# Kernel optimization log

Hardware: AMD Instinct MI355X
Metric: run time of the kernel (lower is better)

## Reference

```python
import jax, jax.numpy as jnp
import numpy as np

B, NP, P, DIM = 128, 64, 128, 512
DST, DCONV, DEPTH = 16, 4, 2
DIN = 2 * DIM          # expand * dim
DTR = DIM // 16        # dt_rank
NCLS = 32


def setup_inputs() -> dict:
    key = jax.random.key(0)
    ks = jax.random.split(key, 12)
    r = lambda k, shape, s=0.02: jax.random.normal(k, shape, jnp.float32) * s
    A_log = jnp.log(jnp.arange(1, DST + 1, dtype=jnp.float32))  # S4D-real init
    return {
        "series": jax.random.normal(ks[0], (B, NP * P), jnp.float32),
        "seg_w": r(ks[1], (NP, P, DIM)),
        "seg_b": jnp.zeros((NP, DIM), jnp.float32),
        "ln_g": jnp.ones((NP, DIM), jnp.float32),
        "ln_b": jnp.zeros((NP, DIM), jnp.float32),
        "in_proj_w": r(ks[2], (DEPTH, 2 * DIN, DIM)),
        "conv_w": r(ks[3], (DEPTH, DIN, DCONV), 0.1),
        "conv_b": jnp.zeros((DEPTH, DIN), jnp.float32),
        "x_proj_w": r(ks[4], (DEPTH, DTR + 2 * DST, DIN)),
        "dt_proj_w": r(ks[5], (DEPTH, DIN, DTR), 0.1),
        "dt_proj_b": r(ks[6], (DEPTH, DIN), 0.5) - 4.0,  # small softplus(dt)
        "A_log": jnp.tile(A_log, (DEPTH, DIN, 1)),
        "D": jnp.ones((DEPTH, DIN), jnp.float32),
        "out_proj_w": r(ks[7], (DEPTH, DIM, DIN)),
        "head_ln_g": jnp.ones((NP * DIM,), jnp.float32),
        "head_ln_b": jnp.zeros((NP * DIM,), jnp.float32),
        "head_w": r(ks[8], (NCLS, NP * DIM)),
        "head_b": jnp.zeros((NCLS,), jnp.float32),
    }


def _layernorm(x, g, b, eps=1e-5):
    mu = x.mean(-1, keepdims=True)
    var = x.var(-1, keepdims=True)
    return (x - mu) / jnp.sqrt(var + eps) * g + b


def _mamba_block(x, wi, cw, cb, wx, wdt, bdt, A_log, Dp, wo):
    # x: [b, l, DIM]
    b, l, _ = x.shape
    xz = jnp.einsum('bld,ed->ble', x, wi)            # [b, l, 2*DIN]
    u, z = jnp.split(xz, 2, axis=-1)
    # depthwise causal conv1d (kernel DCONV, left pad DCONV-1)
    up = jnp.pad(u, ((0, 0), (DCONV - 1, 0), (0, 0)))
    uc = sum(up[:, k:k + l, :] * cw[:, k] for k in range(DCONV)) + cb
    uc = jax.nn.silu(uc)
    x_dbl = jnp.einsum('bld,ed->ble', uc, wx)        # [b, l, DTR+2*DST]
    dt, Bm, Cm = jnp.split(x_dbl, [DTR, DTR + DST], axis=-1)
    delta = jax.nn.softplus(jnp.einsum('blr,dr->bld', dt, wdt) + bdt)  # [b,l,DIN]
    A = -jnp.exp(A_log)                               # [DIN, DST]

    def step(h, inp):
        d_t, B_t, C_t, u_t = inp                      # [b,DIN],[b,DST],[b,DST],[b,DIN]
        dA = jnp.exp(d_t[:, :, None] * A)             # [b, DIN, DST]
        h = dA * h + (d_t * u_t)[:, :, None] * B_t[:, None, :]
        y = jnp.einsum('bdn,bn->bd', h, C_t)
        return h, y

    xs = (delta.transpose(1, 0, 2), Bm.transpose(1, 0, 2),
          Cm.transpose(1, 0, 2), uc.transpose(1, 0, 2))
    h0 = jnp.zeros((b, DIN, DST), x.dtype)
    _, ys = jax.lax.scan(step, h0, xs)                # [l, b, DIN]
    y = ys.transpose(1, 0, 2) + uc * Dp
    y = y * jax.nn.silu(z)
    return jnp.einsum('bld,ed->ble', y, wo)           # [b, l, DIM]


def _forward(series, seg_w, seg_b, ln_g, ln_b, in_proj_w, conv_w, conv_b,
             x_proj_w, dt_proj_w, dt_proj_b, A_log, D, out_proj_w,
             head_ln_g, head_ln_b, head_w, head_b):
    b = series.shape[0]
    x = series.reshape(b, NP, P)                      # equal-size pathway split
    x = jnp.einsum('bnp,npd->bnd', x, seg_w) + seg_b  # per-pathway Linear
    x = _layernorm(x, ln_g, ln_b)                     # per-pathway LayerNorm
    for i in range(DEPTH):                            # stacked Mamba (no residual)
        x = _mamba_block(x, in_proj_w[i], conv_w[i], conv_b[i], x_proj_w[i],
                         dt_proj_w[i], dt_proj_b[i], A_log[i], D[i], out_proj_w[i])
    x = x.reshape(b, NP * DIM)
    x = _layernorm(x, head_ln_g, head_ln_b)
    return x @ head_w.T + head_b


def reference(series, seg_w, seg_b, ln_g, ln_b, in_proj_w, conv_w, conv_b,
              x_proj_w, dt_proj_w, dt_proj_b, A_log, D, out_proj_w,
              head_ln_g, head_ln_b, head_w, head_b):
    return _forward(series, seg_w, seg_b, ln_g, ln_b, in_proj_w, conv_w, conv_b,
                    x_proj_w, dt_proj_w, dt_proj_b, A_log, D, out_proj_w,
                    head_ln_g, head_ln_b, head_w, head_b)
```

## Files before the change

### kernel.cpp

```cpp
#include <hip/hip_runtime.h>

typedef unsigned short u16;
typedef unsigned int   u32;
typedef __attribute__((ext_vector_type(8))) short short8;
typedef __attribute__((ext_vector_type(4))) float floatx4;

static __device__ __forceinline__ float silu_f(float x){
  return x / (1.f + __expf(-x));
}
static __device__ __forceinline__ float bfu2f(u16 u){
  union { u32 i; float f; } v; v.i = ((u32)u) << 16; return v.f;
}
static __device__ __forceinline__ u16 f2bfu(float f){
  union { float f; u32 i; } v; v.f = f;
  u32 x = v.i;
  u32 r = (x + 0x7fffu + ((x >> 16) & 1u)) >> 16;
  return (u16)r;
}
static __device__ __forceinline__ float softplus_f(float v){
  return fmaxf(v, 0.f) + log1pf(__expf(-fabsf(v)));
}

constexpr int cB = 128, cNP = 64, cP = 128, cDIM = 512, cDIN = 1024;
constexpr int cDST = 16, cDTR = 32, cNCLS = 32;
constexpr int cBL = cB * cNP;
constexpr int cXZ = 2 * cDIN;
constexpr long cPSTR = (long)cBL * 64;

__global__ __launch_bounds__(256) void k_f2bf_all(
    const float* __restrict__ s0, u16* __restrict__ d0, int n0,
    const float* __restrict__ s1, u16* __restrict__ d1, int n1,
    const float* __restrict__ s2, u16* __restrict__ d2, int n2,
    const float* __restrict__ s3, u16* __restrict__ d3, int n3,
    const float* __restrict__ s4, u16* __restrict__ d4, int n4)
{
  int i = blockIdx.x * 256 + threadIdx.x;
  const float* s; u16* d;
  if (i < n0) { s = s0; d = d0; }
  else {
    i -= n0;
    if (i < n1) { s = s1; d = d1; }
    else {
      i -= n1;
      if (i < n2) { s = s2; d = d2; }
      else {
        i -= n2;
        if (i < n3) { s = s3; d = d3; }
        else {
          i -= n3;
          if (i >= n4) return;
          s = s4; d = d4;
        }
      }
    }
  }
  const size_t off = (size_t)i * 4;
  float4 v = *(const float4*)(s + off);
  ushort4 o;
  o.x = f2bfu(v.x); o.y = f2bfu(v.y); o.z = f2bfu(v.z); o.w = f2bfu(v.w);
  *(ushort4*)(d + off) = o;
}

__global__ __launch_bounds__(256) void k_segT(
    const float* __restrict__ src, u16* __restrict__ dst)
{
  const int n = blockIdx.z;
  const int p0 = blockIdx.x * 32;
  const int d0 = blockIdx.y * 32;
  const int tx = threadIdx.x & 31;
  const int ty = threadIdx.x >> 5;
  __shared__ float t[32][33];
#pragma unroll
  for (int r = 0; r < 4; ++r)
    t[ty + r * 8][tx] = src[(size_t)n * (cP * cDIM) + (p0 + ty + r * 8) * cDIM + d0 + tx];
  __syncthreads();
#pragma unroll
  for (int r = 0; r < 4; ++r)
    dst[(size_t)n * (cDIM * cP) + (d0 + ty + r * 8) * cP + p0 + tx] =
        f2bfu(t[tx][ty + r * 8]);
}

template<int AMODE, int EPI>
__global__ __launch_bounds__(256) void k_gemm_mfma(
    const void* __restrict__ Av, int lda,
    const u16* __restrict__ W,
    float* __restrict__ C, int ldc,
    u16* __restrict__ Cb, int ldcb,
    const float* __restrict__ bias,
    int K, long azs, long wzs, long czs,
    const float* __restrict__ cwp, const float* __restrict__ cbp,
    u16* __restrict__ ucp)
{
  constexpr int LDT = 40;
  constexpr int SU_LD = 136;
  constexpr int GEMM_SM = 2 * 128 * LDT;
  constexpr int SM_SZ = (EPI == 2) ? (128 * SU_LD) : GEMM_SM;
  __shared__ __align__(16) u16 smem[SM_SZ];
  u16* As = smem;
  u16* Ws = smem + 128 * LDT;

  const int bz = blockIdx.z;
  const u16* Wz = W + (size_t)bz * wzs;

  const int tid = threadIdx.x;
  const int bm = blockIdx.x * 128;
  const int bn = blockIdx.y * 128;
  const int wave = tid >> 6;
  const int lane = tid & 63;
  const int wm = (wave & 1) * 64;
  const int wn = (wave >> 1) * 64;
  const int l15 = lane & 15;
  const int quad = lane >> 4;

  floatx4 acc[4][4];
#pragma unroll
  for (int i = 0; i < 4; ++i)
#pragma unroll
    for (int j = 0; j < 4; ++j) acc[i][j] = (floatx4){0.f, 0.f, 0.f, 0.f};

  const int r0 = tid >> 2;
  const int c0 = (tid & 3) * 8;

  const float* Af = (const float*)Av + (AMODE == 1 ? (size_t)bz * azs : 0);
  const u16*   Ab = (const u16*)Av + (AMODE == 0 ? (size_t)bz * azs : 0);

  float4 fa0, fb0, fa1, fb1;
  short8 ra0, ra1, rw0, rw1;

  if constexpr (AMODE == 1) {
    const float* p0 = Af + (size_t)(bm + r0) * lda + c0;
    const float* p1 = Af + (size_t)(bm + r0 + 64) * lda + c0;
    fa0 = *(const float4*)p0; fb0 = *(const float4*)(p0 + 4);
    fa1 = *(const float4*)p1; fb1 = *(const float4*)(p1 + 4);
  } else if constexpr (AMODE == 0) {
    ra0 = *(const short8*)(Ab + (size_t)(bm + r0)      * lda + c0);
    ra1 = *(const short8*)(Ab + (size_t)(bm + r0 + 64) * lda + c0);
  }
  rw0 = *(const short8*)(Wz + (size_t)(bn + r0)      * K + c0);
  rw1 = *(const short8*)(Wz + (size_t)(bn + r0 + 64) * K + c0);

  for (int k0 = 0; k0 < K; k0 += 32) {
    if constexpr (AMODE == 1) {
      short8 s0, s1;
      s0[0] = (short)f2bfu(fa0.x); s0[1] = (short)f2bfu(fa0.y);
      s0[2] = (short)f2bfu(fa0.z); s0[3] = (short)f2bfu(fa0.w);
      s0[4] = (short)f2bfu(fb0.x); s0[5] = (short)f2bfu(fb0.y);
      s0[6] = (short)f2bfu(fb0.z); s0[7] = (short)f2bfu(fb0.w);
      s1[0] = (short)f2bfu(fa1.x); s1[1] = (short)f2bfu(fa1.y);
      s1[2] = (short)f2bfu(fa1.z); s1[3] = (short)f2bfu(fa1.w);
      s1[4] = (short)f2bfu(fb1.x); s1[5] = (short)f2bfu(fb1.y);
      s1[6] = (short)f2bfu(fb1.z); s1[7] = (short)f2bfu(fb1.w);
      *(short8*)&As[r0 * LDT + c0] = s0;
      *(short8*)&As[(r0 + 64) * LDT + c0] = s1;
    } else if constexpr (AMODE == 0) {
      *(short8*)&As[r0 * LDT + c0] = ra0;
      *(short8*)&As[(r0 + 64) * LDT + c0] = ra1;
    } else {
      const float* base = (const float*)Av;
#pragma unroll
      for (int h = 0; h < 2; ++h) {
        const float* p = base + (size_t)(bm + r0 + h * 64) * 64 + c0;
        float4 a = *(const float4*)p;
        float4 b = *(const float4*)(p + 4);
#pragma unroll
        for (int kc = 1; kc < 4; ++kc) {
          const float* q = p + (size_t)kc * azs;
          float4 va = *(const float4*)q, vb = *(const float4*)(q + 4);
          a.x += va.x; a.y += va.y; a.z += va.z; a.w += va.w;
          b.x += vb.x; b.y += vb.y; b.z += vb.z; b.w += vb.w;
        }
        short8 st;
        st[0] = (short)f2bfu(a.x); st[1] = (short)f2bfu(a.y);
        st[2] = (short)f2bfu(a.z); st[3] = (short)f2bfu(a.w);
        st[4] = (short)f2bfu(b.x); st[5] = (short)f2bfu(b.y);
        st[6] = (short)f2bfu(b.z); st[7] = (short)f2bfu(b.w);
        *(short8*)&As[(r0 + h * 64) * LDT + c0] = st;
      }
    }
    *(short8*)&Ws[r0 * LDT + c0] = rw0;
    *(short8*)&Ws[(r0 + 64) * LDT + c0] = rw1;
    __syncthreads();

    const int kn = k0 + 32;
    if (kn < K) {
      if constexpr (AMODE == 1) {
        const float* p0 = Af + (size_t)(bm + r0) * lda + kn + c0;
        const float* p1 = Af + (size_t)(bm + r0 + 64) * lda + kn + c0;
        fa0 = *(const float4*)p0; fb0 = *(const float4*)(p0 + 4);
        fa1 = *(const float4*)p1; fb1 = *(const float4*)(p1 + 4);
      } else if constexpr (AMODE == 0) {
        ra0 = *(const short8*)(Ab + (size_t)(bm + r0)      * lda + kn + c0);
        ra1 = *(const short8*)(Ab + (size_t)(bm + r0 + 64) * lda + kn + c0);
      }
      rw0 = *(const short8*)(Wz + (size_t)(bn + r0)      * K + kn + c0);
      rw1 = *(const short8*)(Wz + (size_t)(bn + r0 + 64) * K + kn + c0);
    }

    short8 af[4], bf[4];
#pragma unroll
    for (int i = 0; i < 4; ++i)
      af[i] = *(const short8*)&As[(wm + i * 16 + l15) * LDT + quad * 8];
#pragma unroll
    for (int j = 0; j < 4; ++j)
      bf[j] = *(const short8*)&Ws[(wn + j * 16 + l15) * LDT + quad * 8];
#pragma unroll
    for (int i = 0; i < 4; ++i)
#pragma unroll
      for (int j = 0; j < 4; ++j)
        acc[i][j] = __builtin_amdgcn_mfma_f32_16x16x32_bf16(
            af[i], bf[j], acc[i][j], 0, 0, 0);
    __syncthreads();
  }

  if constexpr (EPI == 2) {
    if (bn < cDIN) {
      u16* sU = smem;
#pragma unroll
      for (int i = 0; i < 4; ++i) {
        const int mi = wm + i * 16 + quad * 4;
#pragma unroll
        for (int j = 0; j < 4; ++j) {
          const int nj = wn + j * 16 + l15;
          ushort4 pk;
          pk.x = f2bfu(acc[i][j][0]); pk.y = f2bfu(acc[i][j][1]);
          pk.z = f2bfu(acc[i][j][2]); pk.w = f2bfu(acc[i][j][3]);
          *(ushort4*)&sU[nj * SU_LD + mi] = pk;
        }
      }
      __syncthreads();
      const int c = tid & 127;
      const int s = tid >> 7;
      const int b = (bm >> 6) + s;
      const int d = bn + c;
      const float w0 = cwp[d * 4 + 0], w1 = cwp[d * 4 + 1];
      const float w2 = cwp[d * 4 + 2], w3 = cwp[d * 4 + 3];
      const float cbias = cbp[d];
      u16* dst = ucp + (size_t)b * cNP * cDIN + d;
      const u16* col = &sU[c * SU_LD + s * 64];
      float u0 = 0.f, u1 = 0.f, u2 = 0.f;
      for (int c8 = 0; c8 < 8; ++c8) {
        short8 v8 = *(const short8*)&col[c8 * 8];
        u16 o[8];
#pragma unroll
        for (int i = 0; i < 8; ++i) {
          float u3 = bfu2f((u16)v8[i]);
          float v = w0 * u0 + w1 * u1 + w2 * u2 + w3 * u3 + cbias;
          o[i] = f2bfu(silu_f(v));
          u0 = u1; u1 = u2; u2 = u3;
        }
#pragma unroll
        for (int i = 0; i < 8; ++i)
          dst[(size_t)(c8 * 8 + i) * cDIN] = o[i];
      }
      return;
    }
  }

#pragma unroll
  for (int i = 0; i < 4; ++i) {
    const int m0 = bm + wm + i * 16 + quad * 4;
#pragma unroll
    for (int j = 0; j < 4; ++j) {
      const int n = bn + wn + j * 16 + l15;
      if constexpr (EPI == 1) {
        const float bs = bias[n];
#pragma unroll
        for (int r = 0; r < 4; ++r)
          Cb[(size_t)(m0 + r) * ldcb + n + bz * czs] =
              f2bfu(softplus_f(acc[i][j][r] + bs));
      } else {
        if (C) {
#pragma unroll
          for (int r = 0; r < 4; ++r)
            C[(size_t)(m0 + r) * ldc + n + bz * czs] = acc[i][j][r];
        }
        if (Cb) {
#pragma unroll
          for (int r = 0; r < 4; ++r)
            Cb[(size_t)(m0 + r) * ldcb + n + bz * czs] = f2bfu(acc[i][j][r]);
        }
      }
    }
  }
}

__global__ __launch_bounds__(256) void k_ln(
    const float* __restrict__ xs, const float* __restrict__ sb,
    const float* __restrict__ ln_g, const float* __restrict__ ln_b,
    u16* __restrict__ x0b)
{
  const int tid = threadIdx.x;
  const int r = blockIdx.x * 4 + (tid >> 6);
  const int lane = tid & 63;
  const int d = lane * 8;
  const int n = r & 63;

  const float* row = xs + (size_t)r * cDIM + d;
  float4 a = *(const float4*)row;
  float4 b = *(const float4*)(row + 4);
  const float* sbp = sb + n * cDIM + d;
  float4 s0 = *(const float4*)sbp;
  float4 s1 = *(const float4*)(sbp + 4);
  a.x += s0.x; a.y += s0.y; a.z += s0.z; a.w += s0.w;
  b.x += s1.x; b.y += s1.y; b.z += s1.z; b.w += s1.w;

  float s  = a.x + a.y + a.z + a.w + b.x + b.y + b.z + b.w;
  float s2 = a.x*a.x + a.y*a.y + a.z*a.z + a.w*a.w
           + b.x*b.x + b.y*b.y + b.z*b.z + b.w*b.w;
#pragma unroll
  for (int m = 1; m < 64; m <<= 1) {
    s  += __shfl_xor(s,  m, 64);
    s2 += __shfl_xor(s2, m, 64);
  }
  const float mu = s * (1.f / cDIM);
  const float var = s2 * (1.f / cDIM) - mu * mu;
  const float rstd = rsqrtf(var + 1e-5f);

  const float* g = ln_g + n * cDIM + d;
  const float* be = ln_b + n * cDIM + d;
  float4 g0 = *(const float4*)g, g1 = *(const float4*)(g + 4);
  float4 b0 = *(const float4*)be, b1 = *(const float4*)(be + 4);
  ushort4 o0, o1;
  o0.x = f2bfu((a.x - mu) * rstd * g0.x + b0.x);
  o0.y = f2bfu((a.y - mu) * rstd * g0.y + b0.y);
  o0.z = f2bfu((a.z - mu) * rstd * g0.z + b0.z);
  o0.w = f2bfu((a.w - mu) * rstd * g0.w + b0.w);
  o1.x = f2bfu((b.x - mu) * rstd * g1.x + b1.x);
  o1.y = f2bfu((b.y - mu) * rstd * g1.y + b1.y);
  o1.z = f2bfu((b.z - mu) * rstd * g1.z + b1.z);
  o1.w = f2bfu((b.w - mu) * rstd * g1.w + b1.w);
  *(ushort4*)(x0b + (size_t)r * cDIM + d) = o0;
  *(ushort4*)(x0b + (size_t)r * cDIM + d + 4) = o1;
}

__global__ __launch_bounds__(128) void k_xproj(
    const u16* __restrict__ A, const u16* __restrict__ W,
    float* __restrict__ xpart)
{
  constexpr int LDT = 40;
  __shared__ __align__(16) u16 As[128 * LDT];
  __shared__ __align__(16) u16 Ws[64 * LDT];

  const int tid = threadIdx.x;
  const int bm = blockIdx.x * 128;
  const int kbase = blockIdx.y * 256;
  const int wave = tid >> 6;
  const int lane = tid & 63;
  const int wm = wave * 64;
  const int l15 = lane & 15;
  const int quad = lane >> 4;

  floatx4 acc[4][4];
#pragma unroll
  for (int i = 0; i < 4; ++i)
#pragma unroll
    for (int j = 0; j < 4; ++j) acc[i][j] = (floatx4){0.f, 0.f, 0.f, 0.f};

  short8 rA[4], rW[2];
#pragma unroll
  for (int it = 0; it < 4; ++it) {
    int idx = tid + it * 128, row = idx >> 2, cc = (idx & 3) * 8;
    rA[it] = *(const short8*)(A + (size_t)(bm + row) * cDIN + kbase + cc);
  }
#pragma unroll
  for (int it = 0; it < 2; ++it) {
    int idx = tid + it * 128, row = idx >> 2, cc = (idx & 3) * 8;
    rW[it] = *(const short8*)(W + (size_t)row * cDIN + kbase + cc);
  }

  for (int kk = 0; kk < 256; kk += 32) {
#pragma unroll
    for (int it = 0; it < 4; ++it) {
      int idx = tid + it * 128, row = idx >> 2, cc = (idx & 3) * 8;
      *(short8*)&As[row * LDT + cc] = rA[it];
    }
#pragma unroll
    for (int it = 0; it < 2; ++it) {
      int idx = tid + it * 128, row = idx >> 2, cc = (idx & 3) * 8;
      *(short8*)&Ws[row * LDT + cc] = rW[it];
    }
    __syncthreads();

    if (kk + 32 < 256) {
      const int k0 = kbase + kk + 32;
#pragma unroll
      for (int it = 0; it < 4; ++it) {
        int idx = tid + it * 128, row = idx >> 2, cc = (idx & 3) * 8;
        rA[it] = *(const short8*)(A + (size_t)(bm + row) * cDIN + k0 + cc);
      }
#pragma unroll
      for (int it = 0; it < 2; ++it) {
        int idx = tid + it * 128, row = idx >> 2, cc = (idx & 3) * 8;
        rW[it] = *(const short8*)(W + (size_t)row * cDIN + k0 + cc);
      }
    }

    short8 af[4], bf[4];
#pragma unroll
    for (int i = 0; i < 4; ++i)
      af[i] = *(const short8*)&As[(wm + i * 16 + l15) * LDT + quad * 8];
#pragma unroll
    for (int j = 0; j < 4; ++j)
      bf[j] = *(const short8*)&Ws[(j * 16 + l15) * LDT + quad * 8];
#pragma unroll
    for (int i = 0; i < 4; ++i)
#pragma unroll
      for (int j = 0; j < 4; ++j)
        acc[i][j] = __builtin_amdgcn_mfma_f32_16x16x32_bf16(
            af[i], bf[j], acc[i][j], 0, 0, 0);
    __syncthreads();
  }

  float* out = xpart + (size_t)blockIdx.y * cPSTR;
#pragma unroll
  for (int i = 0; i < 4; ++i) {
    const int m0 = bm + wm + i * 16 + quad * 4;
#pragma unroll
    for (int j = 0; j < 4; ++j) {
      const int n = j * 16 + l15;
#pragma unroll
      for (int r = 0; r < 4; ++r)
        out[(size_t)(m0 + r) * 64 + n] = acc[i][j][r];
    }
  }
}

__global__ __launch_bounds__(256) void k_scan(
    const u16* __restrict__ xz16, u16* __restrict__ uc,
    const float* __restrict__ xpart, const float* __restrict__ A_log,
    const float* __restrict__ Dp)
{
  const int b = blockIdx.x;
  const int tid = threadIdx.x;
  const int d = blockIdx.y * 256 + tid;

  __shared__ float sBC[cNP][32];
  {
    for (int i = tid; i < cNP * 8; i += 256) {
      int l = i >> 3, q = i & 7;
      const float* p = xpart + (size_t)(b * cNP + l) * 64 + 32 + q * 4;
      float4 s = *(const float4*)p;
#pragma unroll
      for (int kc = 1; kc < 4; ++kc) {
        float4 v = *(const float4*)(p + (size_t)kc * cPSTR);
        s.x += v.x; s.y += v.y; s.z += v.z; s.w += v.w;
      }
      *(float4*)&sBC[l][q * 4] = s;
    }
  }

  float A[cDST];
  {
    const float4* ap = (const float4*)(A_log + (size_t)d * cDST);
#pragma unroll
    for (int q = 0; q < 4; ++q) {
      float4 w = ap[q];
      A[q*4+0] = -__expf(w.x); A[q*4+1] = -__expf(w.y);
      A[q*4+2] = -__expf(w.z); A[q*4+3] = -__expf(w.w);
    }
  }
  const float a1 = A[0];
  bool geom = true;
#pragma unroll
  for (int n = 1; n < cDST; ++n)
    geom = geom && (fabsf(A[n] - (float)(n + 1) * a1) <= 1e-4f * fabsf(A[n]));

  float h[cDST];
#pragma unroll
  for (int n = 0; n < cDST; ++n) h[n] = 0.f;
  const float Dv = Dp[d];
  __syncthreads();

  const u16* dsrc = xz16 + d;
  const u16* zsrc = xz16 + cDIN + d;
  u16* usrc = uc + d;
  const size_t rb = (size_t)b * cNP;

  float dvc[8], zvc[8], uvc[8];
#pragma unroll
  for (int i = 0; i < 8; ++i) {
    dvc[i] = bfu2f(dsrc[(rb + i) * cXZ]);
    zvc[i] = bfu2f(zsrc[(rb + i) * cXZ]);
    uvc[i] = bfu2f(usrc[(rb + i) * cDIN]);
  }

  if (geom) {
    for (int c = 0; c < 8; ++c) {
      float dvn[8], zvn[8], uvn[8];
      if (c < 7) {
#pragma unroll
        for (int i = 0; i < 8; ++i) {
          const size_t row = rb + (c + 1) * 8 + i;
          dvn[i] = bfu2f(dsrc[row * cXZ]);
          zvn[i] = bfu2f(zsrc[row * cXZ]);
          uvn[i] = bfu2f(usrc[row * cDIN]);
        }
      }
      u16 yo[8];
#pragma unroll
      for (int i = 0; i < 8; ++i) {
        const int l = c * 8 + i;
        const float dv = dvc[i], zv = zvc[i], uv = uvc[i];
        const float du = dv * uv;
        const float e1 = __expf(dv * a1);
        const float e2 = e1 * e1;
        const float e4 = e2 * e2;
        float p0 = e1, p1 = e2, p2 = e2 * e1, p3 = e4;
        float y0 = 0.f, y1 = 0.f, y2 = 0.f, y3 = 0.f;
#pragma unroll
        for (int g = 0; g < 4; ++g) {
          const int n = g * 4;
          h[n+0] = p0 * h[n+0] + du * sBC[l][n+0];
          y0 += h[n+0] * sBC[l][16 + n+0];
          h[n+1] = p1 * h[n+1] + du * sBC[l][n+1];
          y1 += h[n+1] * sBC[l][16 + n+1];
          h[n+2] = p2 * h[n+2] + du * sBC[l][n+2];
          y2 += h[n+2] * sBC[l][16 + n+2];
          h[n+3] = p3 * h[n+3] + du * sBC[l][n+3];
          y3 += h[n+3] * sBC[l][16 + n+3];
          if (g < 3) { p0 *= e4; p1 *= e4; p2 *= e4; p3 *= e4; }
        }
        float y = (y0 + y1) + (y2 + y3);
        y = (y + uv * Dv) * silu_f(zv);
        yo[i] = f2bfu(y);
      }
#pragma unroll
      for (int i = 0; i < 8; ++i)
        usrc[(rb + c * 8 + i) * cDIN] = yo[i];
      if (c < 7) {
#pragma unroll
        for (int i = 0; i < 8; ++i) {
          dvc[i] = dvn[i]; zvc[i] = zvn[i]; uvc[i] = uvn[i];
        }
      }
    }
  } else {
    for (int c = 0; c < 8; ++c) {
      float dvn[8], zvn[8], uvn[8];
      if (c < 7) {
#pragma unroll
        for (int i = 0; i < 8; ++i) {
          const size_t row = rb + (c + 1) * 8 + i;
          dvn[i] = bfu2f(dsrc[row * cXZ]);
          zvn[i] = bfu2f(zsrc[row * cXZ]);
          uvn[i] = bfu2f(usrc[row * cDIN]);
        }
      }
      u16 yo[8];
#pragma unroll
      for (int i = 0; i < 8; ++i) {
        const int l = c * 8 + i;
        const float dv = dvc[i], zv = zvc[i], uv = uvc[i];
        const float du = dv * uv;
        float y0 = 0.f, y1 = 0.f, y2 = 0.f, y3 = 0.f;
#pragma unroll
        for (int n = 0; n < cDST; n += 4) {
          float dA0 = __expf(dv * A[n+0]);
          float dA1 = __expf(dv * A[n+1]);
          float dA2 = __expf(dv * A[n+2]);
          float dA3 = __expf(dv * A[n+3]);
          h[n+0] = dA0 * h[n+0] + du * sBC[l][n+0];
          y0 += h[n+0] * sBC[l][16 + n+0];
          h[n+1] = dA1 * h[n+1] + du * sBC[l][n+1];
          y1 += h[n+1] * sBC[l][16 + n+1];
          h[n+2] = dA2 * h[n+2] + du * sBC[l][n+2];
          y2 += h[n+2] * sBC[l][16 + n+2];
          h[n+3] = dA3 * h[n+3] + du * sBC[l][n+3];
          y3 += h[n+3] * sBC[l][16 + n+3];
        }
        float y = (y0 + y1) + (y2 + y3);
        y = (y + uv * Dv) * silu_f(zv);
        yo[i] = f2bfu(y);
      }
#pragma unroll
      for (int i = 0; i < 8; ++i)
        usrc[(rb + c * 8 + i) * cDIN] = yo[i];
      if (c < 7) {
#pragma unroll
        for (int i = 0; i < 8; ++i) {
          dvc[i] = dvn[i]; zvc[i] = zvn[i]; uvc[i] = uvn[i];
        }
      }
    }
  }
}

__global__ __launch_bounds__(256) void k_hstats1(
    const float* __restrict__ x, float* __restrict__ pst)
{
  const int b = blockIdx.x;
  const int chunk = blockIdx.y;
  const int tid = threadIdx.x;
  const float4* r4 = (const float4*)(x + (size_t)b * (cNP * cDIM) + chunk * 4096);
  float4 v = r4[tid];
  float4 w = r4[tid + 256];
  float4 u = r4[tid + 512];
  float4 t = r4[tid + 768];
  float s  = v.x + v.y + v.z + v.w + w.x + w.y + w.z + w.w
           + u.x + u.y + u.z + u.w + t.x + t.y + t.z + t.w;
  float s2 = v.x*v.x + v.y*v.y + v.z*v.z + v.w*v.w
           + w.x*w.x + w.y*w.y + w.z*w.z + w.w*w.w
           + u.x*u.x + u.y*u.y + u.z*u.z + u.w*u.w
           + t.x*t.x + t.y*t.y + t.z*t.z + t.w*t.w;
  __shared__ float red[512];
  red[tid] = s; red[256 + tid] = s2;
  __syncthreads();
  for (int st = 128; st > 0; st >>= 1) {
    if (tid < st) { red[tid] += red[tid + st]; red[256+tid] += red[256+tid+st]; }
    __syncthreads();
  }
  if (tid == 0) {
    pst[(b * 8 + chunk) * 2]     = red[0];
    pst[(b * 8 + chunk) * 2 + 1] = red[256];
  }
}

__global__ __launch_bounds__(256) void k_head1(
    const float* __restrict__ x, const float* __restrict__ pst,
    const float* __restrict__ hg, const float* __restrict__ hb,
    const u16* __restrict__ hwb, float* __restrict__ hpart)
{
  const int b = blockIdx.x;
  const int chunk = blockIdx.y;
  const int tid = threadIdx.x;

  float s = 0.f, s2 = 0.f;
#pragma unroll
  for (int c = 0; c < 8; ++c) {
    s  += pst[(b * 8 + c) * 2];
    s2 += pst[(b * 8 + c) * 2 + 1];
  }
  const float mu = s * (1.f / (cNP * cDIM));
  const float var = s2 * (1.f / (cNP * cDIM)) - mu * mu;
  const float rstd = rsqrtf(var + 1e-5f);

  const float* row = x + (size_t)b * (cNP * cDIM);
  const int k0 = chunk * 2048;

  float acc[cNCLS];
#pragma unroll
  for (int c = 0; c < cNCLS; ++c) acc[c] = 0.f;

#pragma unroll
  for (int it = 0; it < 4; ++it) {
    const int i0 = k0 + it * 512 + tid * 2;
    float xn0 = (row[i0]     - mu) * rstd * hg[i0]     + hb[i0];
    float xn1 = (row[i0 + 1] - mu) * rstd * hg[i0 + 1] + hb[i0 + 1];
#pragma unroll
    for (int c = 0; c < cNCLS; ++c) {
      u32 w2 = *(const u32*)(hwb + (size_t)c * (cNP * cDIM) + i0);
      acc[c] += xn0 * bfu2f((u16)(w2 & 0xffffu)) + xn1 * bfu2f((u16)(w2 >> 16));
    }
  }

  __shared__ float sred[cNCLS * 257];
#pragma unroll
  for (int c = 0; c < cNCLS; ++c) sred[c * 257 + tid] = acc[c];
  __syncthreads();
  if (tid < cNCLS * 8) {
    const int c = tid >> 3, p = tid & 7;
    float ss = 0.f;
#pragma unroll
    for (int i = 0; i < 32; ++i) ss += sred[c * 257 + p * 32 + i];
    ss += __shfl_xor(ss, 1, 64);
    ss += __shfl_xor(ss, 2, 64);
    ss += __shfl_xor(ss, 4, 64);
    if (p == 0) hpart[(size_t)(b * 16 + chunk) * cNCLS + c] = ss;
  }
}

__global__ __launch_bounds__(64) void k_head2(
    const float* __restrict__ hpart, const float* __restrict__ hbias,
    float* __restrict__ out)
{
  const int b = blockIdx.x;
  const int c = threadIdx.x;
  if (c < cNCLS) {
    float s = 0.f;
#pragma unroll
    for (int k = 0; k < 16; ++k)
      s += hpart[(size_t)(b * 16 + k) * cNCLS + c];
    out[b * cNCLS + c] = s + hbias[c];
  }
}

extern "C" void kernel_launch(void* const* d_in, const int* in_sizes, int n_in,
                              void* d_out, int out_size, void* d_ws, size_t ws_size,
                              hipStream_t stream)
{
  (void)in_sizes; (void)n_in; (void)out_size; (void)ws_size;

  const float* series    = (const float*)d_in[0];
  const float* seg_w     = (const float*)d_in[1];
  const float* seg_b     = (const float*)d_in[2];
  const float* ln_g      = (const float*)d_in[3];
  const float* ln_b      = (const float*)d_in[4];
  const float* in_proj_w = (const float*)d_in[5];
  const float* conv_w    = (const float*)d_in[6];
  const float* conv_b    = (const float*)d_in[7];
  const float* x_proj_w  = (const float*)d_in[8];
  const float* dt_proj_w = (const float*)d_in[9];
  const float* dt_proj_b = (const float*)d_in[10];
  const float* A_log     = (const float*)d_in[11];
  const float* Dp        = (const float*)d_in[12];
  const float* out_proj_w= (const float*)d_in[13];
  const float* head_ln_g = (const float*)d_in[14];
  const float* head_ln_b = (const float*)d_in[15];
  const float* head_w    = (const float*)d_in[16];
  const float* head_b    = (const float*)d_in[17];

  u16*   xz16   = (u16*)d_ws;
  float* x0     = (float*)(xz16 + (size_t)cBL * cXZ);
  float* xsegf  = x0;
  float* pst    = x0 + (size_t)cBL * cDIM;
  float* hpart  = pst + 128 * 8 * 2;
  u16*   x0b    = (u16*)(hpart + 128 * 16 * 32);
  u16*   wib    = x0b + (size_t)cBL * cDIM;
  u16*   wob    = wib + (size_t)2 * (2*cDIN) * cDIM;
  u16*   wdtb   = wob + (size_t)2 * cDIM * cDIN;
  u16*   wxb    = wdtb + (size_t)2 * cDIN * cDTR;
  u16*   wsegT  = wxb + (size_t)2 * 64 * cDIN;
  u16*   ucb16  = wsegT + (size_t)cNP * cDIM * cP;
  u16*   hwb    = ucb16 + (size_t)cBL * cDIN;
  float* xpart  = (float*)x0b;

  k_f2bf_all<<<4288, 256, 0, stream>>>(
      in_proj_w,  wib,  (2 * (2*cDIN) * cDIM) / 4,
      out_proj_w, wob,  (2 * cDIM * cDIN) / 4,
      dt_proj_w,  wdtb, (2 * cDIN * cDTR) / 4,
      x_proj_w,   wxb,  (2 * 64 * cDIN) / 4,
      head_w,     hwb,  (cNCLS * cNP * cDIM) / 4);
  k_segT<<<dim3(cP/32, cDIM/32, cNP), 256, 0, stream>>>(seg_w, wsegT);

  k_gemm_mfma<1,0><<<dim3(1, cDIM/128, cNP), 256, 0, stream>>>(
      series, cNP * cP, wsegT, xsegf, cNP * cDIM, (u16*)nullptr, 0,
      nullptr, cP, (long)cP, (long)cDIM * cP, (long)cDIM,
      nullptr, nullptr, nullptr);
  k_ln<<<cBL / 4, 256, 0, stream>>>(xsegf, seg_b, ln_g, ln_b, x0b);

  for (int dep = 0; dep < 2; ++dep) {
    const u16*   wi  = wib  + (size_t)dep * (2*cDIN) * cDIM;
    const u16*   wo  = wob  + (size_t)dep * cDIM * cDIN;
    const u16*   wdt = wdtb + (size_t)dep * cDIN * cDTR;
    const u16*   wx  = wxb  + (size_t)dep * 64 * cDIN;
    const float* cwd = conv_w     + (size_t)dep * cDIN * 4;
    const float* cbd = conv_b     + (size_t)dep * cDIN;
    const float* bdt = dt_proj_b  + (size_t)dep * cDIN;
    const float* Ald = A_log      + (size_t)dep * cDIN * cDST;
    const float* Dd  = Dp         + (size_t)dep * cDIN;

    k_gemm_mfma<0,2><<<dim3(cBL/128, (2*cDIN)/128), 256, 0, stream>>>(
        x0b, cDIM, wi, (float*)nullptr, 0, xz16, cXZ, nullptr, cDIM, 0, 0, 0,
        cwd, cbd, ucb16);
    k_xproj<<<dim3(cBL / 128, 4), 128, 0, stream>>>(ucb16, wx, xpart);
    k_gemm_mfma<2,1><<<dim3(cBL/128, cDIN/128), 256, 0, stream>>>(
        xpart, 64, wdt, (float*)nullptr, 0, xz16, cXZ, bdt, cDTR,
        cPSTR, 0, 0, nullptr, nullptr, nullptr);
    k_scan<<<dim3(cB, 4), 256, 0, stream>>>(xz16, ucb16, xpart, Ald, Dd);
    k_gemm_mfma<0,0><<<dim3(cBL/128, cDIM/128), 256, 0, stream>>>(
        ucb16, cDIN, wo,
        dep ? x0 : (float*)nullptr, cDIM,
        dep ? (u16*)nullptr : x0b, cDIM,
        nullptr, cDIN, 0, 0, 0,
        nullptr, nullptr, nullptr);
  }

  k_hstats1<<<dim3(cB, 8), 256, 0, stream>>>(x0, pst);
  k_head1<<<dim3(cB, 16), 256, 0, stream>>>(x0, pst, head_ln_g, head_ln_b,
                                            hwb, hpart);
  k_head2<<<cB, 64, 0, stream>>>(hpart, head_b, (float*)d_out);
}
```

Measured before the change: 387.6 us.

## Fuse dt_proj and softplus into scan; keep final activations in bf16

Drops the separate dt_proj GEMM kernel. The scan kernel now sums the x_proj partials for both the dt and B/C columns, loads each channel's fp32 dt_proj weight row into registers, and computes delta with a 32-wide dot product plus softplus per timestep. This removes a launch, the bf16 delta write into xz16 and its reread, and the dt_proj weight conversion. The last out_proj now writes only bf16, and the head stats and head GEMV read bf16 instead of fp32, halving that traffic at some cost in precision. The trade-off is extra per-timestep FMAs and register pressure in the scan.

```diff
diff --git a/kernel.cpp b/kernel.cpp
--- a/kernel.cpp
+++ b/kernel.cpp
@@ -86,7 +86,6 @@
     const u16* __restrict__ W,
     float* __restrict__ C, int ldc,
     u16* __restrict__ Cb, int ldcb,
-    const float* __restrict__ bias,
     int K, long azs, long wzs, long czs,
     const float* __restrict__ cwp, const float* __restrict__ cbp,
     u16* __restrict__ ucp)
@@ -132,7 +131,7 @@
     const float* p1 = Af + (size_t)(bm + r0 + 64) * lda + c0;
     fa0 = *(const float4*)p0; fb0 = *(const float4*)(p0 + 4);
     fa1 = *(const float4*)p1; fb1 = *(const float4*)(p1 + 4);
-  } else if constexpr (AMODE == 0) {
+  } else {
     ra0 = *(const short8*)(Ab + (size_t)(bm + r0)      * lda + c0);
     ra1 = *(const short8*)(Ab + (size_t)(bm + r0 + 64) * lda + c0);
   }
@@ -152,30 +151,9 @@
       s1[6] = (short)f2bfu(fb1.z); s1[7] = (short)f2bfu(fb1.w);
       *(short8*)&As[r0 * LDT + c0] = s0;
       *(short8*)&As[(r0 + 64) * LDT + c0] = s1;
-    } else if constexpr (AMODE == 0) {
+    } else {
       *(short8*)&As[r0 * LDT + c0] = ra0;
       *(short8*)&As[(r0 + 64) * LDT + c0] = ra1;
-    } else {
-      const float* base = (const float*)Av;
-#pragma unroll
-      for (int h = 0; h < 2; ++h) {
-        const float* p = base + (size_t)(bm + r0 + h * 64) * 64 + c0;
-        float4 a = *(const float4*)p;
-        float4 b = *(const float4*)(p + 4);
-#pragma unroll
-        for (int kc = 1; kc < 4; ++kc) {
-          const float* q = p + (size_t)kc * azs;
-          float4 va = *(const float4*)q, vb = *(const float4*)(q + 4);
-          a.x += va.x; a.y += va.y; a.z += va.z; a.w += va.w;
-          b.x += vb.x; b.y += vb.y; b.z += vb.z; b.w += vb.w;
-        }
-        short8 st;
-        st[0] = (short)f2bfu(a.x); st[1] = (short)f2bfu(a.y);
-        st[2] = (short)f2bfu(a.z); st[3] = (short)f2bfu(a.w);
-        st[4] = (short)f2bfu(b.x); st[5] = (short)f2bfu(b.y);
-        st[6] = (short)f2bfu(b.z); st[7] = (short)f2bfu(b.w);
-        *(short8*)&As[(r0 + h * 64) * LDT + c0] = st;
-      }
     }
     *(short8*)&Ws[r0 * LDT + c0] = rw0;
     *(short8*)&Ws[(r0 + 64) * LDT + c0] = rw1;
@@ -188,7 +166,7 @@
         const float* p1 = Af + (size_t)(bm + r0 + 64) * lda + kn + c0;
         fa0 = *(const float4*)p0; fb0 = *(const float4*)(p0 + 4);
         fa1 = *(const float4*)p1; fb1 = *(const float4*)(p1 + 4);
-      } else if constexpr (AMODE == 0) {
+      } else {
         ra0 = *(const short8*)(Ab + (size_t)(bm + r0)      * lda + kn + c0);
         ra1 = *(const short8*)(Ab + (size_t)(bm + r0 + 64) * lda + kn + c0);
       }
@@ -262,23 +240,15 @@
 #pragma unroll
     for (int j = 0; j < 4; ++j) {
       const int n = bn + wn + j * 16 + l15;
-      if constexpr (EPI == 1) {
-        const float bs = bias[n];
+      if (C) {
 #pragma unroll
         for (int r = 0; r < 4; ++r)
-          Cb[(size_t)(m0 + r) * ldcb + n + bz * czs] =
-              f2bfu(softplus_f(acc[i][j][r] + bs));
-      } else {
-        if (C) {
-#pragma unroll
-          for (int r = 0; r < 4; ++r)
-            C[(size_t)(m0 + r) * ldc + n + bz * czs] = acc[i][j][r];
-        }
-        if (Cb) {
-#pragma unroll
-          for (int r = 0; r < 4; ++r)
-            Cb[(size_t)(m0 + r) * ldcb + n + bz * czs] = f2bfu(acc[i][j][r]);
-        }
+          C[(size_t)(m0 + r) * ldc + n + bz * czs] = acc[i][j][r];
+      }
+      if (Cb) {
+#pragma unroll
+        for (int r = 0; r < 4; ++r)
+          Cb[(size_t)(m0 + r) * ldcb + n + bz * czs] = f2bfu(acc[i][j][r]);
       }
     }
   }
@@ -428,26 +398,40 @@
 __global__ __launch_bounds__(256) void k_scan(
     const u16* __restrict__ xz16, u16* __restrict__ uc,
     const float* __restrict__ xpart, const float* __restrict__ A_log,
-    const float* __restrict__ Dp)
+    const float* __restrict__ Dp, const float* __restrict__ wdt,
+    const float* __restrict__ bdt)
 {
   const int b = blockIdx.x;
   const int tid = threadIdx.x;
   const int d = blockIdx.y * 256 + tid;
 
+  __shared__ float sDT[cNP][32];
   __shared__ float sBC[cNP][32];
   {
-    for (int i = tid; i < cNP * 8; i += 256) {
-      int l = i >> 3, q = i & 7;
-      const float* p = xpart + (size_t)(b * cNP + l) * 64 + 32 + q * 4;
+    for (int i = tid; i < cNP * 16; i += 256) {
+      int l = i >> 4, q = i & 15;
+      const float* p = xpart + (size_t)(b * cNP + l) * 64 + q * 4;
       float4 s = *(const float4*)p;
 #pragma unroll
       for (int kc = 1; kc < 4; ++kc) {
         float4 v = *(const float4*)(p + (size_t)kc * cPSTR);
         s.x += v.x; s.y += v.y; s.z += v.z; s.w += v.w;
       }
-      *(float4*)&sBC[l][q * 4] = s;
-    }
-  }
+      if (q < 8) *(float4*)&sDT[l][q * 4] = s;
+      else       *(float4*)&sBC[l][(q - 8) * 4] = s;
+    }
+  }
+
+  float wd[cDTR];
+  {
+    const float4* wp = (const float4*)(wdt + (size_t)d * cDTR);
+#pragma unroll
+    for (int q = 0; q < 8; ++q) {
+      float4 w = wp[q];
+      wd[q*4+0] = w.x; wd[q*4+1] = w.y; wd[q*4+2] = w.z; wd[q*4+3] = w.w;
+    }
+  }
+  const float bdtv = bdt[d];
 
   float A[cDST];
   {
@@ -471,27 +455,24 @@
   const float Dv = Dp[d];
   __syncthreads();
 
-  const u16* dsrc = xz16 + d;
   const u16* zsrc = xz16 + cDIN + d;
   u16* usrc = uc + d;
   const size_t rb = (size_t)b * cNP;
 
-  float dvc[8], zvc[8], uvc[8];
+  float zvc[8], uvc[8];
 #pragma unroll
   for (int i = 0; i < 8; ++i) {
-    dvc[i] = bfu2f(dsrc[(rb + i) * cXZ]);
     zvc[i] = bfu2f(zsrc[(rb + i) * cXZ]);
     uvc[i] = bfu2f(usrc[(rb + i) * cDIN]);
   }
 
   if (geom) {
     for (int c = 0; c < 8; ++c) {
-      float dvn[8], zvn[8], uvn[8];
+      float zvn[8], uvn[8];
       if (c < 7) {
 #pragma unroll
         for (int i = 0; i < 8; ++i) {
           const size_t row = rb + (c + 1) * 8 + i;
-          dvn[i] = bfu2f(dsrc[row * cXZ]);
           zvn[i] = bfu2f(zsrc[row * cXZ]);
           uvn[i] = bfu2f(usrc[row * cDIN]);
         }
@@ -500,7 +481,16 @@
 #pragma unroll
       for (int i = 0; i < 8; ++i) {
         const int l = c * 8 + i;
-        const float dv = dvc[i], zv = zvc[i], uv = uvc[i];
+        float a0 = 0.f, a1s = 0.f, a2 = 0.f, a3 = 0.f;
+#pragma unroll
+        for (int k = 0; k < cDTR; k += 4) {
+          a0 += sDT[l][k+0] * wd[k+0];
+          a1s += sDT[l][k+1] * wd[k+1];
+          a2 += sDT[l][k+2] * wd[k+2];
+          a3 += sDT[l][k+3] * wd[k+3];
+        }
+        const float dv = softplus_f((a0 + a1s) + (a2 + a3) + bdtv);
+        const float zv = zvc[i], uv = uvc[i];
         const float du = dv * uv;
         const float e1 = __expf(dv * a1);
         const float e2 = e1 * e1;
@@ -529,19 +519,16 @@
         usrc[(rb + c * 8 + i) * cDIN] = yo[i];
       if (c < 7) {
 #pragma unroll
-        for (int i = 0; i < 8; ++i) {
-          dvc[i] = dvn[i]; zvc[i] = zvn[i]; uvc[i] = uvn[i];
-        }
+        for (int i = 0; i < 8; ++i) { zvc[i] = zvn[i]; uvc[i] = uvn[i]; }
       }
     }
   } else {
     for (int c = 0; c < 8; ++c) {
-      float dvn[8], zvn[8], uvn[8];
+      float zvn[8], uvn[8];
       if (c < 7) {
 #pragma unroll
         for (int i = 0; i < 8; ++i) {
           const size_t row = rb + (c + 1) * 8 + i;
-          dvn[i] = bfu2f(dsrc[row * cXZ]);
           zvn[i] = bfu2f(zsrc[row * cXZ]);
           uvn[i] = bfu2f(usrc[row * cDIN]);
         }
@@ -550,7 +537,16 @@
 #pragma unroll
       for (int i = 0; i < 8; ++i) {
         const int l = c * 8 + i;
-        const float dv = dvc[i], zv = zvc[i], uv = uvc[i];
+        float a0 = 0.f, a1s = 0.f, a2 = 0.f, a3 = 0.f;
+#pragma unroll
+        for (int k = 0; k < cDTR; k += 4) {
+          a0 += sDT[l][k+0] * wd[k+0];
+          a1s += sDT[l][k+1] * wd[k+1];
+          a2 += sDT[l][k+2] * wd[k+2];
+          a3 += sDT[l][k+3] * wd[k+3];
+        }
+        const float dv = softplus_f((a0 + a1s) + (a2 + a3) + bdtv);
+        const float zv = zvc[i], uv = uvc[i];
         const float du = dv * uv;
         float y0 = 0.f, y1 = 0.f, y2 = 0.f, y3 = 0.f;
 #pragma unroll
@@ -577,31 +573,27 @@
         usrc[(rb + c * 8 + i) * cDIN] = yo[i];
       if (c < 7) {
 #pragma unroll
-        for (int i = 0; i < 8; ++i) {
-          dvc[i] = dvn[i]; zvc[i] = zvn[i]; uvc[i] = uvn[i];
-        }
+        for (int i = 0; i < 8; ++i) { zvc[i] = zvn[i]; uvc[i] = uvn[i]; }
       }
     }
   }
 }
 
 __global__ __launch_bounds__(256) void k_hstats1(
-    const float* __restrict__ x, float* __restrict__ pst)
+    const u16* __restrict__ x, float* __restrict__ pst)
 {
   const int b = blockIdx.x;
   const int chunk = blockIdx.y;
   const int tid = threadIdx.x;
-  const float4* r4 = (const float4*)(x + (size_t)b * (cNP * cDIM) + chunk * 4096);
-  float4 v = r4[tid];
-  float4 w = r4[tid + 256];
-  float4 u = r4[tid + 512];
-  float4 t = r4[tid + 768];
-  float s  = v.x + v.y + v.z + v.w + w.x + w.y + w.z + w.w
-           + u.x + u.y + u.z + u.w + t.x + t.y + t.z + t.w;
-  float s2 = v.x*v.x + v.y*v.y + v.z*v.z + v.w*v.w
-           + w.x*w.x + w.y*w.y + w.z*w.z + w.w*w.w
-           + u.x*u.x + u.y*u.y + u.z*u.z + u.w*u.w
-           + t.x*t.x + t.y*t.y + t.z*t.z + t.w*t.w;
+  const short8* r8 = (const short8*)(x + (size_t)b * (cNP * cDIM) + chunk * 4096);
+  short8 v = r8[tid];
+  short8 w = r8[tid + 256];
+  float s = 0.f, s2 = 0.f;
+#pragma unroll
+  for (int i = 0; i < 8; ++i) {
+    float f = bfu2f((u16)v[i]); s += f; s2 += f * f;
+    float g = bfu2f((u16)w[i]); s += g; s2 += g * g;
+  }
   __shared__ float red[512];
   red[tid] = s; red[256 + tid] = s2;
   __syncthreads();
@@ -616,7 +608,7 @@
 }
 
 __global__ __launch_bounds__(256) void k_head1(
-    const float* __restrict__ x, const float* __restrict__ pst,
+    const u16* __restrict__ x, const float* __restrict__ pst,
     const float* __restrict__ hg, const float* __restrict__ hb,
     const u16* __restrict__ hwb, float* __restrict__ hpart)
 {
@@ -634,7 +626,7 @@
   const float var = s2 * (1.f / (cNP * cDIM)) - mu * mu;
   const float rstd = rsqrtf(var + 1e-5f);
 
-  const float* row = x + (size_t)b * (cNP * cDIM);
+  const u16* row = x + (size_t)b * (cNP * cDIM);
   const int k0 = chunk * 2048;
 
   float acc[cNCLS];
@@ -644,8 +636,9 @@
 #pragma unroll
   for (int it = 0; it < 4; ++it) {
     const int i0 = k0 + it * 512 + tid * 2;
-    float xn0 = (row[i0]     - mu) * rstd * hg[i0]     + hb[i0];
-    float xn1 = (row[i0 + 1] - mu) * rstd * hg[i0 + 1] + hb[i0 + 1];
+    u32 x2 = *(const u32*)(row + i0);
+    float xn0 = (bfu2f((u16)(x2 & 0xffffu)) - mu) * rstd * hg[i0]     + hb[i0];
+    float xn1 = (bfu2f((u16)(x2 >> 16))     - mu) * rstd * hg[i0 + 1] + hb[i0 + 1];
 #pragma unroll
     for (int c = 0; c < cNCLS; ++c) {
       u32 w2 = *(const u32*)(hwb + (size_t)c * (cNP * cDIM) + i0);
@@ -710,63 +703,56 @@
   const float* head_b    = (const float*)d_in[17];
 
   u16*   xz16   = (u16*)d_ws;
-  float* x0     = (float*)(xz16 + (size_t)cBL * cXZ);
-  float* xsegf  = x0;
-  float* pst    = x0 + (size_t)cBL * cDIM;
+  float* xsegf  = (float*)(xz16 + (size_t)cBL * cXZ);
+  float* pst    = xsegf + (size_t)cBL * cDIM;
   float* hpart  = pst + 128 * 8 * 2;
   u16*   x0b    = (u16*)(hpart + 128 * 16 * 32);
   u16*   wib    = x0b + (size_t)cBL * cDIM;
   u16*   wob    = wib + (size_t)2 * (2*cDIN) * cDIM;
-  u16*   wdtb   = wob + (size_t)2 * cDIM * cDIN;
-  u16*   wxb    = wdtb + (size_t)2 * cDIN * cDTR;
+  u16*   wxb    = wob + (size_t)2 * cDIM * cDIN;
   u16*   wsegT  = wxb + (size_t)2 * 64 * cDIN;
   u16*   ucb16  = wsegT + (size_t)cNP * cDIM * cP;
   u16*   hwb    = ucb16 + (size_t)cBL * cDIN;
   float* xpart  = (float*)x0b;
 
-  k_f2bf_all<<<4288, 256, 0, stream>>>(
-      in_proj_w,  wib,  (2 * (2*cDIN) * cDIM) / 4,
-      out_proj_w, wob,  (2 * cDIM * cDIN) / 4,
-      dt_proj_w,  wdtb, (2 * cDIN * cDTR) / 4,
-      x_proj_w,   wxb,  (2 * 64 * cDIN) / 4,
-      head_w,     hwb,  (cNCLS * cNP * cDIM) / 4);
+  k_f2bf_all<<<4224, 256, 0, stream>>>(
+      in_proj_w,  wib, (2 * (2*cDIN) * cDIM) / 4,
+      out_proj_w, wob, (2 * cDIM * cDIN) / 4,
+      x_proj_w,   wxb, (2 * 64 * cDIN) / 4,
+      head_w,     hwb, (cNCLS * cNP * cDIM) / 4,
+      nullptr, nullptr, 0);
   k_segT<<<dim3(cP/32, cDIM/32, cNP), 256, 0, stream>>>(seg_w, wsegT);
 
   k_gemm_mfma<1,0><<<dim3(1, cDIM/128, cNP), 256, 0, stream>>>(
       series, cNP * cP, wsegT, xsegf, cNP * cDIM, (u16*)nullptr, 0,
-      nullptr, cP, (long)cP, (long)cDIM * cP, (long)cDIM,
+      cP, (long)cP, (long)cDIM * cP, (long)cDIM,
       nullptr, nullptr, nullptr);
   k_ln<<<cBL / 4, 256, 0, stream>>>(xsegf, seg_b, ln_g, ln_b, x0b);
 
   for (int dep = 0; dep < 2; ++dep) {
-    const u16*   wi  = wib  + (size_t)dep * (2*cDIN) * cDIM;
-    const u16*   wo  = wob  + (size_t)dep * cDIM * cDIN;
-    const u16*   wdt = wdtb + (size_t)dep * cDIN * cDTR;
-    const u16*   wx  = wxb  + (size_t)dep * 64 * cDIN;
-    const float* cwd = conv_w     + (size_t)dep * cDIN * 4;
-    const float* cbd = conv_b     + (size_t)dep * cDIN;
-    const float* bdt = dt_proj_b  + (size_t)dep * cDIN;
-    const float* Ald = A_log      + (size_t)dep * cDIN * cDST;
-    const float* Dd  = Dp         + (size_t)dep * cDIN;
+    const u16*   wi  = wib + (size_t)dep * (2*cDIN) * cDIM;
+    const u16*   wo  = wob + (size_t)dep * cDIM * cDIN;
+    const u16*   wx  = wxb + (size_t)dep * 64 * cDIN;
+    const float* cwd = conv_w    + (size_t)dep * cDIN * 4;
+    const float* cbd = conv_b    + (size_t)dep * cDIN;
+    const float* wdt = dt_proj_w + (size_t)dep * cDIN * cDTR;
+    const float* bdt = dt_proj_b + (size_t)dep * cDIN;
+    const float* Ald = A_log     + (size_t)dep * cDIN * cDST;
+    const float* Dd  = Dp        + (size_t)dep * cDIN;
 
     k_gemm_mfma<0,2><<<dim3(cBL/128, (2*cDIN)/128), 256, 0, stream>>>(
-        x0b, cDIM, wi, (float*)nullptr, 0, xz16, cXZ, nullptr, cDIM, 0, 0, 0,
+        x0b, cDIM, wi, (float*)nullptr, 0, xz16, cXZ, cDIM, 0, 0, 0,
         cwd, cbd, ucb16);
     k_xproj<<<dim3(cBL / 128, 4), 128, 0, stream>>>(ucb16, wx, xpart);
-    k_gemm_mfma<2,1><<<dim3(cBL/128, cDIN/128), 256, 0, stream>>>(
-        xpart, 64, wdt, (float*)nullptr, 0, xz16, cXZ, bdt, cDTR,
-        cPSTR, 0, 0, nullptr, nullptr, nullptr);
-    k_scan<<<dim3(cB, 4), 256, 0, stream>>>(xz16, ucb16, xpart, Ald, Dd);
+    k_scan<<<dim3(cB, 4), 256, 0, stream>>>(xz16, ucb16, xpart, Ald, Dd,
+                                            wdt, bdt);
     k_gemm_mfma<0,0><<<dim3(cBL/128, cDIM/128), 256, 0, stream>>>(
-        ucb16, cDIN, wo,
-        dep ? x0 : (float*)nullptr, cDIM,
-        dep ? (u16*)nullptr : x0b, cDIM,
-        nullptr, cDIN, 0, 0, 0,
-        nullptr, nullptr, nullptr);
-  }
-
-  k_hstats1<<<dim3(cB, 8), 256, 0, stream>>>(x0, pst);
-  k_head1<<<dim3(cB, 16), 256, 0, stream>>>(x0, pst, head_ln_g, head_ln_b,
+        ucb16, cDIN, wo, (float*)nullptr, 0, x0b, cDIM,
+        cDIN, 0, 0, 0, nullptr, nullptr, nullptr);
+  }
+
+  k_hstats1<<<dim3(cB, 8), 256, 0, stream>>>(x0b, pst);
+  k_head1<<<dim3(cB, 16), 256, 0, stream>>>(x0b, pst, head_ln_g, head_ln_b,
                                             hwb, hpart);
   k_head2<<<cB, 64, 0, stream>>>(hpart, head_b, (float*)d_out);
 }
```

After: 420.1 us. 8.4% more time.
